# Kernel optimization log

Measured on AMD Instinct MI355X. Metric: run time of the kernel, lower is better.

## Reference

```python
import jax, jax.numpy as jnp
import numpy as np

HEADS = 8
DIM_HEAD = 64


def setup_inputs() -> dict:
    key = jax.random.key(0)
    ks = jax.random.split(key, 4)
    B, C, H, W = 1, 256, 64, 64
    inner = HEADS * DIM_HEAD  # 512
    x = jax.random.normal(ks[0], (B, C, H, W), dtype=jnp.float32)
    norm_w = jnp.ones((C,), dtype=jnp.float32)                      # RMSNorm weight (1,C,1,1) flattened
    w_qkv = jax.random.normal(ks[1], (3 * inner, C), dtype=jnp.float32) * 0.02  # 1x1 conv, no bias
    w_out = jax.random.normal(ks[2], (C, inner), dtype=jnp.float32) * 0.02      # 1x1 conv
    b_out = jax.random.normal(ks[3], (C,), dtype=jnp.float32) * 0.02
    return {"x": x, "norm_w": norm_w, "w_qkv": w_qkv, "w_out": w_out, "b_out": b_out}


def reference(x, norm_w, w_qkv, w_out, b_out):
    B, C, H, W = x.shape
    N = H * W
    # RMSNorm: F.normalize over channel dim (L2, eps clamp) * weight * sqrt(C)
    l2 = jnp.sqrt(jnp.sum(x * x, axis=1, keepdims=True))
    xn = x / jnp.maximum(l2, 1e-12) * norm_w[None, :, None, None] * (C ** 0.5)
    # 1x1 conv QKV = channel matmul
    qkv = jnp.einsum('oc,bchw->bohw', w_qkv, xn)  # [B, 3*inner, H, W]
    q, k, v = jnp.split(qkv, 3, axis=1)

    def split_heads(t):
        # 'b (h d) x y -> b h (x y) d'
        return t.reshape(B, HEADS, DIM_HEAD, N).transpose(0, 1, 3, 2)

    q, k, v = map(split_heads, (q, k, v))
    scale = DIM_HEAD ** -0.5
    scores = jnp.einsum('bhnd,bhmd->bhnm', q, k) * scale  # [B,H,N,N]
    attn = jax.nn.softmax(scores, axis=-1)
    out = jnp.einsum('bhnm,bhmd->bhnd', attn, v)
    # 'b h (x y) d -> b (h d) x y'
    out = out.transpose(0, 1, 3, 2).reshape(B, HEADS * DIM_HEAD, H, W)
    # output 1x1 conv + residual (note: residual is the NORMALIZED x, per source)
    return jnp.einsum('ci,bihw->bchw', w_out, out) + b_out[None, :, None, None] + xn
```

## Files before the change

kernel.cpp:

```cpp
#include <hip/hip_runtime.h>


#define NPIX 4096
#define CIN 256
#define INNER 512
#define NHEAD 8
#define DH 64

typedef _Float16 f16;
typedef __attribute__((ext_vector_type(8))) _Float16 f16x8;
typedef __attribute__((ext_vector_type(4))) float f32x4;

static __device__ __forceinline__ f32x4 mfma_f16(f16x8 a, f16x8 b, f32x4 c) {
  return __builtin_amdgcn_mfma_f32_16x16x32_f16(a, b, c, 0, 0, 0);
}

static __device__ __forceinline__ unsigned pk2(float lo, float hi) {
  return __builtin_bit_cast(unsigned, __builtin_amdgcn_cvt_pkrtz(lo, hi));
}

static __device__ __forceinline__ void gload_lds16(const void* g, void* l) {
  __builtin_amdgcn_global_load_lds(
      (const __attribute__((address_space(1))) unsigned*)g,
      (__attribute__((address_space(3))) unsigned*)l, 16, 0, 0);
}

__global__ __launch_bounds__(256) void k_cvt2(const float* __restrict__ a1, int n1,
                                              const float* __restrict__ a2, int n2,
                                              f16* __restrict__ b) {
  int i = blockIdx.x * 256 + threadIdx.x;
  if (i < n1) b[i] = (f16)a1[i];
  else if (i < n1 + n2) b[i] = (f16)a2[i - n1];
}

__global__ __launch_bounds__(256) void k_rmsnorm(const float* __restrict__ x,
                                                 const float* __restrict__ w,
                                                 float* __restrict__ xn,
                                                 f16* __restrict__ xnT) {
  const int pi = threadIdx.x & 15, cs = threadIdx.x >> 4;
  const int p = blockIdx.x * 16 + pi;
  __shared__ float red[16][16];
  float xv[16];
  float ss = 0.f;
#pragma unroll
  for (int i = 0; i < 16; ++i) {
    xv[i] = x[(cs * 16 + i) * NPIX + p];
    ss += xv[i] * xv[i];
  }
  red[cs][pi] = ss;
  __syncthreads();
  float tot = 0.f;
#pragma unroll
  for (int s = 0; s < 16; ++s) tot += red[s][pi];
  float inv = 16.0f / fmaxf(sqrtf(tot), 1e-12f);
  union { f16x8 v[2]; f16 h[16]; } hv;
#pragma unroll
  for (int i = 0; i < 16; ++i) {
    int c = cs * 16 + i;
    float v = xv[i] * inv * w[c];
    xn[c * NPIX + p] = v;
    hv.h[i] = (f16)v;
  }
  *(f16x8*)(xnT + (size_t)p * CIN + cs * 16) = hv.v[0];
  *(f16x8*)(xnT + (size_t)p * CIN + cs * 16 + 8) = hv.v[1];
}

__global__ __launch_bounds__(256) void k_qkv(const f16* __restrict__ wqkv,
                                             const f16* __restrict__ xnT,
                                             f16* __restrict__ qT,
                                             f16* __restrict__ kT,
                                             f16* __restrict__ vv) {
  const int lane = threadIdx.x & 63, wave = threadIdx.x >> 6;
  const int l15 = lane & 15, quad = lane >> 4;
  const int obase = blockIdx.y * 64 + (wave >> 1) * 32;
  const int pbase = blockIdx.x * 128 + (wave & 1) * 64;
  const int sect = blockIdx.y >> 3;
  f32x4 acc[8];
#pragma unroll
  for (int i = 0; i < 8; ++i) acc[i] = (f32x4){0.f, 0.f, 0.f, 0.f};
#pragma unroll
  for (int kc = 0; kc < CIN / 32; ++kc) {
    f16x8 af[2], bfr[4];
#pragma unroll
    for (int oc = 0; oc < 2; ++oc)
      af[oc] = *(const f16x8*)(wqkv + (size_t)(obase + oc * 16 + l15) * CIN + kc * 32 + quad * 8);
#pragma unroll
    for (int pc = 0; pc < 4; ++pc)
      bfr[pc] = *(const f16x8*)(xnT + (size_t)(pbase + pc * 16 + l15) * CIN + kc * 32 + quad * 8);
    if (sect < 2) {
#pragma unroll
      for (int pc = 0; pc < 4; ++pc)
#pragma unroll
        for (int oc = 0; oc < 2; ++oc)
          acc[pc * 2 + oc] = mfma_f16(bfr[pc], af[oc], acc[pc * 2 + oc]);
    } else {
#pragma unroll
      for (int oc = 0; oc < 2; ++oc)
#pragma unroll
        for (int pc = 0; pc < 4; ++pc)
          acc[oc * 4 + pc] = mfma_f16(af[oc], bfr[pc], acc[oc * 4 + pc]);
    }
  }
  if (sect < 2) {
    f16* dst = (sect == 0) ? qT : kT;
    const float sc = (sect == 0) ? 0.18033688f : 1.0f;
    const int head = blockIdx.y & 7;
    const int dd = (wave >> 1) * 32;
#pragma unroll
    for (int pc = 0; pc < 4; ++pc)
#pragma unroll
      for (int oc = 0; oc < 2; ++oc)
#pragma unroll
        for (int r = 0; r < 4; ++r) {
          int p = pbase + pc * 16 + quad * 4 + r;
          dst[((size_t)(head << 12) + p) * DH + dd + oc * 16 + l15] =
              (f16)(acc[pc * 2 + oc][r] * sc);
        }
  } else {
#pragma unroll
    for (int oc = 0; oc < 2; ++oc)
#pragma unroll
      for (int r = 0; r < 4; ++r) {
        int o = obase + oc * 16 + quad * 4 + r - 2 * INNER;
#pragma unroll
        for (int pc = 0; pc < 4; ++pc)
          vv[(size_t)o * NPIX + pbase + pc * 16 + l15] = (f16)acc[oc * 4 + pc][r];
      }
  }
}

template <typename PT>
__global__ __launch_bounds__(256, 2) void k_attn(const f16* __restrict__ qT,
                                                 const f16* __restrict__ kT,
                                                 const f16* __restrict__ vv,
                                                 PT* __restrict__ Opart,
                                                 float* __restrict__ Lpart) {
  const int bid = blockIdx.x;
  const int head = bid & 7, split = (bid >> 3) & 3, qb = bid >> 5;
  const int tid = threadIdx.x;
  const int wave = tid >> 6, lane = tid & 63;
  const int l15 = lane & 15, quad = lane >> 4;
  const int keybase = split * 1024;

  __shared__ f16 KV[2][8192];

  const int qrow = (head << 12) + qb * 256 + wave * 64;
  f16x8 qf[4][2];
#pragma unroll
  for (int qt = 0; qt < 4; ++qt)
#pragma unroll
    for (int kc = 0; kc < 2; ++kc)
      qf[qt][kc] = *(const f16x8*)(qT + (size_t)(qrow + qt * 16 + l15) * DH + kc * 32 + quad * 8);

  f32x4 o[4][4];
  float ol[4] = {0.f, 0.f, 0.f, 0.f};
#pragma unroll
  for (int qt = 0; qt < 4; ++qt)
#pragma unroll
    for (int c = 0; c < 4; ++c) o[qt][c] = (f32x4){0.f, 0.f, 0.f, 0.f};

  const int rx = l15 & 7;
  const bool qodd = (quad & 1) != 0;

  const int sRow8 = lane >> 3, sCol = lane & 7;
  const f16* sp[4];
  const int step = (wave < 2) ? 64 * DH : 64;
#pragma unroll
  for (int j = 0; j < 4; ++j) {
    const int Rb = wave * 4096 + j * 1024;
    if (wave < 2) {
      const int key = (Rb >> 7) + sRow8;
      sp[j] = kT + ((size_t)(head << 12) + keybase + key) * DH + ((sCol ^ (key & 7)) << 3);
    } else {
      const int dd = ((Rb - 8192) >> 7) + sRow8;
      sp[j] = vv + ((size_t)(head * DH) + dd) * NPIX + keybase + ((sCol ^ (dd & 7)) << 3);
    }
  }
  auto stage = [&](int b) {
    char* base = (char*)(&KV[b][0]) + wave * 4096;
#pragma unroll
    for (int j = 0; j < 4; ++j) {
      gload_lds16(sp[j], base + j * 1024);
      sp[j] += step;
    }
  };

  stage(0);
  __syncthreads();

  for (int ch = 0; ch < 16; ++ch) {
    const int b = ch & 1;
    if (ch < 15) stage(b ^ 1);
    const f16* Kb = &KV[b][0];
    const f16* Vb = &KV[b][4096];
#pragma unroll
    for (int h = 0; h < 2; ++h) {
      f16x8 kf[2][2], vf[4];
#pragma unroll
      for (int nc = 0; nc < 2; ++nc) {
        const int key = h * 32 + nc * 16 + l15;
#pragma unroll
        for (int kc = 0; kc < 2; ++kc)
          kf[nc][kc] = *(const f16x8*)(Kb + key * 64 + (((kc * 4 + quad) ^ rx) << 3));
      }
#pragma unroll
      for (int c = 0; c < 4; ++c) {
        const int dd = c * 16 + l15;
        vf[c] = *(const f16x8*)(Vb + dd * 64 + (((h * 4 + quad) ^ rx) << 3));
      }
#pragma unroll
      for (int qt = 0; qt < 4; ++qt) {
        f32x4 s0 = mfma_f16(kf[0][0], qf[qt][0], (f32x4){0.f, 0.f, 0.f, 0.f});
        s0 = mfma_f16(kf[0][1], qf[qt][1], s0);
        f32x4 s1 = mfma_f16(kf[1][0], qf[qt][0], (f32x4){0.f, 0.f, 0.f, 0.f});
        s1 = mfma_f16(kf[1][1], qf[qt][1], s1);
        float p0[4], p1[4];
#pragma unroll
        for (int r = 0; r < 4; ++r) {
          p0[r] = __builtin_amdgcn_exp2f(s0[r]);
          p1[r] = __builtin_amdgcn_exp2f(s1[r]);
        }
        ol[qt] += ((p0[0] + p0[1]) + (p0[2] + p0[3])) +
                  ((p1[0] + p1[1]) + (p1[2] + p1[3]));
        unsigned A0 = pk2(p0[0], p0[1]), B0 = pk2(p0[2], p0[3]);
        unsigned A1 = pk2(p1[0], p1[1]), B1 = pk2(p1[2], p1[3]);
        asm("v_permlane16_swap_b32 %0, %1" : "+v"(A0), "+v"(A1));
        asm("v_permlane16_swap_b32 %0, %1" : "+v"(B0), "+v"(B1));
        unsigned xa = A0, ya = A0;
        asm("v_permlane32_swap_b32 %0, %1" : "+v"(xa), "+v"(ya));
        unsigned xa2 = A1, ya2 = A1;
        asm("v_permlane32_swap_b32 %0, %1" : "+v"(xa2), "+v"(ya2));
        unsigned xb = B0, yb = B0;
        asm("v_permlane32_swap_b32 %0, %1" : "+v"(xb), "+v"(yb));
        unsigned xb2 = B1, yb2 = B1;
        asm("v_permlane32_swap_b32 %0, %1" : "+v"(xb2), "+v"(yb2));
        union { f16x8 v; unsigned u[4]; } pf;
        pf.u[0] = qodd ? ya : xa;
        pf.u[1] = qodd ? yb : xb;
        pf.u[2] = qodd ? ya2 : xa2;
        pf.u[3] = qodd ? yb2 : xb2;
#pragma unroll
        for (int c = 0; c < 4; ++c) o[qt][c] = mfma_f16(vf[c], pf.v, o[qt][c]);
      }
    }
    __syncthreads();
  }

#pragma unroll
  for (int qt = 0; qt < 4; ++qt) {
    ol[qt] += __shfl_xor(ol[qt], 16);
    ol[qt] += __shfl_xor(ol[qt], 32);
  }

#pragma unroll
  for (int qt = 0; qt < 4; ++qt) {
#pragma unroll
    for (int c = 0; c < 4; ++c) {
      const size_t off =
          ((size_t)split * 32768 + qrow + qt * 16 + l15) * 64 + c * 16 + quad * 4;
      if constexpr (sizeof(PT) == 4) {
        *(float4*)(Opart + off) =
            make_float4(o[qt][c][0], o[qt][c][1], o[qt][c][2], o[qt][c][3]);
      } else {
#pragma unroll
        for (int r = 0; r < 4; ++r) Opart[off + r] = (PT)o[qt][c][r];
      }
    }
    if (quad == 0) Lpart[split * 32768 + qrow + qt * 16 + l15] = ol[qt];
  }
}

template <typename PT>
__global__ __launch_bounds__(256) void k_merge(const PT* __restrict__ Opart,
                                               const float* __restrict__ Lpart,
                                               f16* __restrict__ Ows) {
  const int tg = blockIdx.x * 256 + threadIdx.x;
  const int qi = tg >> 2;
  const size_t base = (size_t)tg * 16;
  float acc[16];
#pragma unroll
  for (int i = 0; i < 16; ++i) acc[i] = 0.f;
  float L = 0.f;
#pragma unroll
  for (int s = 0; s < 4; ++s) {
    const PT* p = Opart + (size_t)s * (32768 * 64) + base;
    if constexpr (sizeof(PT) == 4) {
      const float4* p4 = (const float4*)p;
      float4 v0 = p4[0], v1 = p4[1], v2 = p4[2], v3 = p4[3];
      acc[0] += v0.x; acc[1] += v0.y; acc[2] += v0.z; acc[3] += v0.w;
      acc[4] += v1.x; acc[5] += v1.y; acc[6] += v1.z; acc[7] += v1.w;
      acc[8] += v2.x; acc[9] += v2.y; acc[10] += v2.z; acc[11] += v2.w;
      acc[12] += v3.x; acc[13] += v3.y; acc[14] += v3.z; acc[15] += v3.w;
    } else {
      const f16x8* ph = (const f16x8*)p;
      f16x8 v0 = ph[0], v1 = ph[1];
#pragma unroll
      for (int i = 0; i < 8; ++i) {
        acc[i] += (float)v0[i];
        acc[8 + i] += (float)v1[i];
      }
    }
    L += Lpart[s * 32768 + qi];
  }
  union { f16x8 v[2]; f16 h[16]; } hv;
#pragma unroll
  for (int i = 0; i < 16; ++i) hv.h[i] = (f16)(acc[i] / L);
  *(f16x8*)(Ows + base) = hv.v[0];
  *(f16x8*)(Ows + base + 8) = hv.v[1];
}

__global__ __launch_bounds__(256) void k_oproj(const f16* __restrict__ wout,
                                               const f16* __restrict__ Ows,
                                               const float* __restrict__ bout,
                                               const float* __restrict__ xn,
                                               float* __restrict__ out) {
  const int lane = threadIdx.x & 63, wave = threadIdx.x >> 6;
  const int l15 = lane & 15, quad = lane >> 4;
  const int mbase = blockIdx.y * 32 + (wave >> 1) * 16;
  const int pbase = blockIdx.x * 64 + (wave & 1) * 32;
  f32x4 acc[2];
  acc[0] = (f32x4){0.f, 0.f, 0.f, 0.f};
  acc[1] = (f32x4){0.f, 0.f, 0.f, 0.f};
#pragma unroll
  for (int kc = 0; kc < INNER / 32; ++kc) {
    f16x8 af = *(const f16x8*)(wout + (size_t)(mbase + l15) * INNER + kc * 32 + quad * 8);
    int i0 = kc * 32 + quad * 8;
    int head = i0 >> 6, d0 = i0 & 63;
#pragma unroll
    for (int pc = 0; pc < 2; ++pc) {
      f16x8 bfr = *(const f16x8*)(Ows + ((size_t)(head << 12) + pbase + pc * 16 + l15) * DH + d0);
      acc[pc] = mfma_f16(af, bfr, acc[pc]);
    }
  }
#pragma unroll
  for (int pc = 0; pc < 2; ++pc)
#pragma unroll
    for (int r = 0; r < 4; ++r) {
      int c = mbase + quad * 4 + r, p = pbase + pc * 16 + l15;
      out[c * NPIX + p] = acc[pc][r] + bout[c] + xn[c * NPIX + p];
    }
}

extern "C" void kernel_launch(void* const* d_in, const int* in_sizes, int n_in,
                              void* d_out, int out_size, void* d_ws, size_t ws_size,
                              hipStream_t stream) {
  (void)in_sizes; (void)n_in; (void)out_size;
  const float* x      = (const float*)d_in[0];
  const float* norm_w = (const float*)d_in[1];
  const float* w_qkv  = (const float*)d_in[2];
  const float* w_out  = (const float*)d_in[3];
  const float* b_out  = (const float*)d_in[4];
  float* out = (float*)d_out;

  char* ws = (char*)d_ws;
  float* xn    = (float*)(ws);
  f16* xnT     = (f16*)(ws + (4u << 20));
  f16* qT      = (f16*)(ws + (6u << 20));
  f16* kT      = (f16*)(ws + (10u << 20));
  f16* vv      = (f16*)(ws + (14u << 20));
  f16* Ows     = (f16*)(ws + (18u << 20));
  f16* wqkv_h  = (f16*)(ws + (22u << 20));
  f16* wout_h  = (f16*)(ws + (22u << 20) + 786432);

  const int n1 = 3 * INNER * CIN, n2 = CIN * INNER;
  hipLaunchKernelGGL(k_cvt2, dim3((n1 + n2 + 255) / 256), dim3(256), 0, stream,
                     w_qkv, n1, w_out, n2, wqkv_h);
  hipLaunchKernelGGL(k_rmsnorm, dim3(NPIX / 16), dim3(256), 0, stream, x, norm_w, xn, xnT);
  hipLaunchKernelGGL(k_qkv, dim3(NPIX / 128, 1536 / 64), dim3(256), 0, stream,
                     wqkv_h, xnT, qT, kT, vv);

  const size_t OPLANE = (size_t)32768 * 64;
  char* pbase = ws + (24u << 20);
  if (ws_size >= (24u << 20) + OPLANE * 4 * sizeof(float) + 4 * 32768 * sizeof(float)) {
    float* Op = (float*)pbase;
    float* Lp = (float*)(pbase + OPLANE * 4 * sizeof(float));
    hipLaunchKernelGGL((k_attn<float>), dim3(512), dim3(256), 0, stream,
                       qT, kT, vv, Op, Lp);
    hipLaunchKernelGGL((k_merge<float>), dim3(512), dim3(256), 0, stream,
                       Op, Lp, Ows);
  } else {
    f16* Op = (f16*)pbase;
    float* Lp = (float*)(pbase + OPLANE * 4 * sizeof(f16));
    hipLaunchKernelGGL((k_attn<f16>), dim3(512), dim3(256), 0, stream,
                       qT, kT, vv, Op, Lp);
    hipLaunchKernelGGL((k_merge<f16>), dim3(512), dim3(256), 0, stream,
                       Op, Lp, Ows);
  }

  hipLaunchKernelGGL(k_oproj, dim3(NPIX / 64, CIN / 32), dim3(256), 0, stream,
                     wout_h, Ows, b_out, xn, out);
}
```

Baseline: 153.4 us.

## Halve attention query tile, fuse prep kernels, use fp16 partial outputs

The attention kernel now gives each wave 32 query rows instead of 64 and launches 1024 blocks with a 4-blocks-per-SM launch bound, so more blocks can be resident and the grid covers the GPU better. The cost is that each K/V tile loaded into shared memory is reused across fewer queries. Split-K partial outputs are always stored as fp16, which cuts the write and read traffic between attention and merge at some precision cost. RMSNorm and the weight conversion are fused into one launch, and merge multiplies by a reciprocal instead of dividing.

```diff
diff --git a/kernel.cpp b/kernel.cpp
--- a/kernel.cpp
+++ b/kernel.cpp
@@ -9,6 +9,7 @@
 
 typedef _Float16 f16;
 typedef __attribute__((ext_vector_type(8))) _Float16 f16x8;
+typedef __attribute__((ext_vector_type(4))) _Float16 f16x4;
 typedef __attribute__((ext_vector_type(4))) float f32x4;
 
 static __device__ __forceinline__ f32x4 mfma_f16(f16x8 a, f16x8 b, f32x4 c) {
@@ -25,44 +26,43 @@
       (__attribute__((address_space(3))) unsigned*)l, 16, 0, 0);
 }
 
-__global__ __launch_bounds__(256) void k_cvt2(const float* __restrict__ a1, int n1,
-                                              const float* __restrict__ a2, int n2,
-                                              f16* __restrict__ b) {
-  int i = blockIdx.x * 256 + threadIdx.x;
-  if (i < n1) b[i] = (f16)a1[i];
-  else if (i < n1 + n2) b[i] = (f16)a2[i - n1];
-}
-
-__global__ __launch_bounds__(256) void k_rmsnorm(const float* __restrict__ x,
-                                                 const float* __restrict__ w,
-                                                 float* __restrict__ xn,
-                                                 f16* __restrict__ xnT) {
-  const int pi = threadIdx.x & 15, cs = threadIdx.x >> 4;
-  const int p = blockIdx.x * 16 + pi;
-  __shared__ float red[16][16];
-  float xv[16];
-  float ss = 0.f;
-#pragma unroll
-  for (int i = 0; i < 16; ++i) {
-    xv[i] = x[(cs * 16 + i) * NPIX + p];
-    ss += xv[i] * xv[i];
-  }
-  red[cs][pi] = ss;
-  __syncthreads();
-  float tot = 0.f;
-#pragma unroll
-  for (int s = 0; s < 16; ++s) tot += red[s][pi];
-  float inv = 16.0f / fmaxf(sqrtf(tot), 1e-12f);
-  union { f16x8 v[2]; f16 h[16]; } hv;
-#pragma unroll
-  for (int i = 0; i < 16; ++i) {
-    int c = cs * 16 + i;
-    float v = xv[i] * inv * w[c];
-    xn[c * NPIX + p] = v;
-    hv.h[i] = (f16)v;
-  }
-  *(f16x8*)(xnT + (size_t)p * CIN + cs * 16) = hv.v[0];
-  *(f16x8*)(xnT + (size_t)p * CIN + cs * 16 + 8) = hv.v[1];
+__global__ __launch_bounds__(256) void k_prep(
+    const float* __restrict__ x, const float* __restrict__ w,
+    float* __restrict__ xn, f16* __restrict__ xnT,
+    const float* __restrict__ w1, int n1,
+    const float* __restrict__ w2, int n2, f16* __restrict__ wh) {
+  const int b = blockIdx.x;
+  if (b < NPIX / 8) {
+    const int pi = threadIdx.x & 7, cs = threadIdx.x >> 3;
+    const int p = b * 8 + pi;
+    __shared__ float red[32][8];
+    float xv[8];
+    float ss = 0.f;
+#pragma unroll
+    for (int i = 0; i < 8; ++i) {
+      xv[i] = x[(cs * 8 + i) * NPIX + p];
+      ss += xv[i] * xv[i];
+    }
+    red[cs][pi] = ss;
+    __syncthreads();
+    float tot = 0.f;
+#pragma unroll
+    for (int s = 0; s < 32; ++s) tot += red[s][pi];
+    float inv = 16.0f / fmaxf(sqrtf(tot), 1e-12f);
+    union { f16x8 v; f16 h[8]; } hv;
+#pragma unroll
+    for (int i = 0; i < 8; ++i) {
+      int c = cs * 8 + i;
+      float v = xv[i] * inv * w[c];
+      xn[c * NPIX + p] = v;
+      hv.h[i] = (f16)v;
+    }
+    *(f16x8*)(xnT + (size_t)p * CIN + cs * 8) = hv.v;
+  } else {
+    int i = (b - NPIX / 8) * 256 + threadIdx.x;
+    if (i < n1) wh[i] = (f16)w1[i];
+    else if (i < n1 + n2) wh[i] = (f16)w2[i - n1];
+  }
 }
 
 __global__ __launch_bounds__(256) void k_qkv(const f16* __restrict__ wqkv,
@@ -129,11 +129,10 @@
   }
 }
 
-template <typename PT>
-__global__ __launch_bounds__(256, 2) void k_attn(const f16* __restrict__ qT,
+__global__ __launch_bounds__(256, 4) void k_attn(const f16* __restrict__ qT,
                                                  const f16* __restrict__ kT,
                                                  const f16* __restrict__ vv,
-                                                 PT* __restrict__ Opart,
+                                                 f16* __restrict__ Opart,
                                                  float* __restrict__ Lpart) {
   const int bid = blockIdx.x;
   const int head = bid & 7, split = (bid >> 3) & 3, qb = bid >> 5;
@@ -144,18 +143,18 @@
 
   __shared__ f16 KV[2][8192];
 
-  const int qrow = (head << 12) + qb * 256 + wave * 64;
-  f16x8 qf[4][2];
-#pragma unroll
-  for (int qt = 0; qt < 4; ++qt)
+  const int qrow = (head << 12) + qb * 128 + wave * 32;
+  f16x8 qf[2][2];
+#pragma unroll
+  for (int qt = 0; qt < 2; ++qt)
 #pragma unroll
     for (int kc = 0; kc < 2; ++kc)
       qf[qt][kc] = *(const f16x8*)(qT + (size_t)(qrow + qt * 16 + l15) * DH + kc * 32 + quad * 8);
 
-  f32x4 o[4][4];
-  float ol[4] = {0.f, 0.f, 0.f, 0.f};
-#pragma unroll
-  for (int qt = 0; qt < 4; ++qt)
+  f32x4 o[2][4];
+  float ol[2] = {0.f, 0.f};
+#pragma unroll
+  for (int qt = 0; qt < 2; ++qt)
 #pragma unroll
     for (int c = 0; c < 4; ++c) o[qt][c] = (f32x4){0.f, 0.f, 0.f, 0.f};
 
@@ -209,7 +208,7 @@
         vf[c] = *(const f16x8*)(Vb + dd * 64 + (((h * 4 + quad) ^ rx) << 3));
       }
 #pragma unroll
-      for (int qt = 0; qt < 4; ++qt) {
+      for (int qt = 0; qt < 2; ++qt) {
         f32x4 s0 = mfma_f16(kf[0][0], qf[qt][0], (f32x4){0.f, 0.f, 0.f, 0.f});
         s0 = mfma_f16(kf[0][1], qf[qt][1], s0);
         f32x4 s1 = mfma_f16(kf[1][0], qf[qt][0], (f32x4){0.f, 0.f, 0.f, 0.f});
@@ -247,31 +246,26 @@
   }
 
 #pragma unroll
-  for (int qt = 0; qt < 4; ++qt) {
+  for (int qt = 0; qt < 2; ++qt) {
     ol[qt] += __shfl_xor(ol[qt], 16);
     ol[qt] += __shfl_xor(ol[qt], 32);
   }
 
 #pragma unroll
-  for (int qt = 0; qt < 4; ++qt) {
+  for (int qt = 0; qt < 2; ++qt) {
 #pragma unroll
     for (int c = 0; c < 4; ++c) {
       const size_t off =
           ((size_t)split * 32768 + qrow + qt * 16 + l15) * 64 + c * 16 + quad * 4;
-      if constexpr (sizeof(PT) == 4) {
-        *(float4*)(Opart + off) =
-            make_float4(o[qt][c][0], o[qt][c][1], o[qt][c][2], o[qt][c][3]);
-      } else {
-#pragma unroll
-        for (int r = 0; r < 4; ++r) Opart[off + r] = (PT)o[qt][c][r];
-      }
+      f16x4 hv = {(f16)o[qt][c][0], (f16)o[qt][c][1], (f16)o[qt][c][2],
+                  (f16)o[qt][c][3]};
+      *(f16x4*)(Opart + off) = hv;
     }
     if (quad == 0) Lpart[split * 32768 + qrow + qt * 16 + l15] = ol[qt];
   }
 }
 
-template <typename PT>
-__global__ __launch_bounds__(256) void k_merge(const PT* __restrict__ Opart,
+__global__ __launch_bounds__(256) void k_merge(const f16* __restrict__ Opart,
                                                const float* __restrict__ Lpart,
                                                f16* __restrict__ Ows) {
   const int tg = blockIdx.x * 256 + threadIdx.x;
@@ -283,28 +277,19 @@
   float L = 0.f;
 #pragma unroll
   for (int s = 0; s < 4; ++s) {
-    const PT* p = Opart + (size_t)s * (32768 * 64) + base;
-    if constexpr (sizeof(PT) == 4) {
-      const float4* p4 = (const float4*)p;
-      float4 v0 = p4[0], v1 = p4[1], v2 = p4[2], v3 = p4[3];
-      acc[0] += v0.x; acc[1] += v0.y; acc[2] += v0.z; acc[3] += v0.w;
-      acc[4] += v1.x; acc[5] += v1.y; acc[6] += v1.z; acc[7] += v1.w;
-      acc[8] += v2.x; acc[9] += v2.y; acc[10] += v2.z; acc[11] += v2.w;
-      acc[12] += v3.x; acc[13] += v3.y; acc[14] += v3.z; acc[15] += v3.w;
-    } else {
-      const f16x8* ph = (const f16x8*)p;
-      f16x8 v0 = ph[0], v1 = ph[1];
-#pragma unroll
-      for (int i = 0; i < 8; ++i) {
-        acc[i] += (float)v0[i];
-        acc[8 + i] += (float)v1[i];
-      }
+    const f16x8* ph = (const f16x8*)(Opart + (size_t)s * (32768 * 64) + base);
+    f16x8 v0 = ph[0], v1 = ph[1];
+#pragma unroll
+    for (int i = 0; i < 8; ++i) {
+      acc[i] += (float)v0[i];
+      acc[8 + i] += (float)v1[i];
     }
     L += Lpart[s * 32768 + qi];
   }
+  const float rL = 1.0f / L;
   union { f16x8 v[2]; f16 h[16]; } hv;
 #pragma unroll
-  for (int i = 0; i < 16; ++i) hv.h[i] = (f16)(acc[i] / L);
+  for (int i = 0; i < 16; ++i) hv.h[i] = (f16)(acc[i] * rL);
   *(f16x8*)(Ows + base) = hv.v[0];
   *(f16x8*)(Ows + base + 8) = hv.v[1];
 }
@@ -344,7 +329,7 @@
 extern "C" void kernel_launch(void* const* d_in, const int* in_sizes, int n_in,
                               void* d_out, int out_size, void* d_ws, size_t ws_size,
                               hipStream_t stream) {
-  (void)in_sizes; (void)n_in; (void)out_size;
+  (void)in_sizes; (void)n_in; (void)out_size; (void)ws_size;
   const float* x      = (const float*)d_in[0];
   const float* norm_w = (const float*)d_in[1];
   const float* w_qkv  = (const float*)d_in[2];
@@ -361,32 +346,17 @@
   f16* Ows     = (f16*)(ws + (18u << 20));
   f16* wqkv_h  = (f16*)(ws + (22u << 20));
   f16* wout_h  = (f16*)(ws + (22u << 20) + 786432);
+  f16* Opart   = (f16*)(ws + (24u << 20));
+  float* Lpart = (float*)(ws + (40u << 20));
 
   const int n1 = 3 * INNER * CIN, n2 = CIN * INNER;
-  hipLaunchKernelGGL(k_cvt2, dim3((n1 + n2 + 255) / 256), dim3(256), 0, stream,
-                     w_qkv, n1, w_out, n2, wqkv_h);
-  hipLaunchKernelGGL(k_rmsnorm, dim3(NPIX / 16), dim3(256), 0, stream, x, norm_w, xn, xnT);
+  hipLaunchKernelGGL(k_prep, dim3(NPIX / 8 + (n1 + n2 + 255) / 256), dim3(256), 0,
+                     stream, x, norm_w, xn, xnT, w_qkv, n1, w_out, n2, wqkv_h);
   hipLaunchKernelGGL(k_qkv, dim3(NPIX / 128, 1536 / 64), dim3(256), 0, stream,
                      wqkv_h, xnT, qT, kT, vv);
-
-  const size_t OPLANE = (size_t)32768 * 64;
-  char* pbase = ws + (24u << 20);
-  if (ws_size >= (24u << 20) + OPLANE * 4 * sizeof(float) + 4 * 32768 * sizeof(float)) {
-    float* Op = (float*)pbase;
-    float* Lp = (float*)(pbase + OPLANE * 4 * sizeof(float));
-    hipLaunchKernelGGL((k_attn<float>), dim3(512), dim3(256), 0, stream,
-                       qT, kT, vv, Op, Lp);
-    hipLaunchKernelGGL((k_merge<float>), dim3(512), dim3(256), 0, stream,
-                       Op, Lp, Ows);
-  } else {
-    f16* Op = (f16*)pbase;
-    float* Lp = (float*)(pbase + OPLANE * 4 * sizeof(f16));
-    hipLaunchKernelGGL((k_attn<f16>), dim3(512), dim3(256), 0, stream,
-                       qT, kT, vv, Op, Lp);
-    hipLaunchKernelGGL((k_merge<f16>), dim3(512), dim3(256), 0, stream,
-                       Op, Lp, Ows);
-  }
-
+  hipLaunchKernelGGL(k_attn, dim3(1024), dim3(256), 0, stream,
+                     qT, kT, vv, Opart, Lpart);
+  hipLaunchKernelGGL(k_merge, dim3(512), dim3(256), 0, stream, Opart, Lpart, Ows);
   hipLaunchKernelGGL(k_oproj, dim3(NPIX / 64, CIN / 32), dim3(256), 0, stream,
                      wout_h, Ows, b_out, xn, out);
 }
```

Result: no change. 151.0 us (-1.6%).
